# Kernel optimization log

Measured on AMD Instinct MI355X. Metric: run time of the kernel, lower is better.

The kernel has to match this reference:

```python
import jax, jax.numpy as jnp
import numpy as np

B, N, NB, E, H, A, K, D = 32, 512, 10, 1024, 256, 82, 4, 3


def setup_inputs() -> dict:
    key = jax.random.key(0)
    ks = iter(jax.random.split(key, 64))
    f = lambda shape: jax.random.normal(next(ks), shape, jnp.float32) * 0.05
    inp = {
        "atom_fea": jax.random.normal(next(ks), (B, N, A), jnp.float32),
        "bond_fea": jax.random.normal(next(ks), (B, E, 6), jnp.float32),
        "d_anb": jax.random.randint(next(ks), (B, N, NB), 0, N),
        "d_bnb": jax.random.randint(next(ks), (B, N, NB), 0, E),
        "d_nbs_mask": (jax.random.uniform(next(ks), (B, N, NB)) < 0.8).astype(jnp.float32),
        "d_mask": (jax.random.uniform(next(ks), (B, N)) < 0.9).astype(jnp.float32),
        "Wv": f((A, H)), "bv": f((H,)),
        "Wa_main": f((D, K, H, H)), "ba_main": f((D, K, H)),
        "Wa_super": f((D, K, H, H)), "ba_super": f((D, K, H)),
        "Wm": f((D, K, H, H)), "bm": f((D, K, H)),
        "Wbmm": f((D, K, H)), "bbmm": f((D, K)),
        "Wm2s": f((D, K * H, H)), "bm2s": f((D, H)),
        "Ws2m": f((D, H, H)), "bs2m": f((D, H)),
        "Wsup": f((D, H, H)), "bsup": f((D, H)),
        "Wzm1": f((D, H, H)), "bzm1": f((D, H)),
        "Wzm2": f((D, H, H)), "bzm2": f((D, H)),
        "Wzs1": f((D, H, H)), "bzs1": f((D, H)),
        "Wzs2": f((D, H, H)), "bzs2": f((D, H)),
        "Wu2": f((D, H + 6, H)), "bu2": f((D, H)),
        "Wu1": f((D, 2 * H, H)), "bu1": f((D, H)),
    }
    return inp


def mask_softmax(a, mask):
    a_max = jnp.max(a, -1, keepdims=True)
    e = jnp.exp(a - a_max) * mask
    return e / (jnp.sum(e, -1, keepdims=True) + 1e-6)


def _forward(atom_fea, bond_fea, d_nbs_mask, d_mask,
             Wv, bv, Wa_main, ba_main, Wa_super, ba_super, Wm, bm, Wbmm, bbmm,
             Wm2s, bm2s, Ws2m, bs2m, Wsup, bsup,
             Wzm1, bzm1, Wzm2, bzm2, Wzs1, bzs1, Wzs2, bzs2,
             Wu2, bu2, Wu1, bu1, d_anb, d_bnb):
    Bn = atom_fea.shape[0]
    bidx = jnp.arange(Bn)[:, None, None]
    # vertex embedding (default leaky_relu slope 0.01)
    vf = jax.nn.leaky_relu(atom_fea @ Wv + bv, 0.01)            # [B,N,H]
    sf = jnp.sum(vf * d_mask[:, :, None], axis=1, keepdims=True)  # [B,1,H]
    mask3 = d_nbs_mask[..., None]                               # [B,N,NB,1]
    for d in range(D):
        # --- multi-head main->super attention (vectorized over heads k) ---
        a_main = jnp.tanh(jnp.einsum('bnh,khj->bknj', vf, Wa_main[d]) + ba_main[d][None, :, None, :])
        a_super = jnp.tanh(jnp.einsum('boh,khj->bkoj', sf, Wa_super[d]) + ba_super[d][None, :, None, :])
        a = jnp.einsum('bknh,kh->bkn', a_main * a_super, Wbmm[d]) + bbmm[d][None, :, None]
        attn = mask_softmax(a, d_mask[:, None, :])               # [B,K,N]
        mvf = jnp.einsum('bnh,khj->bknj', vf, Wm[d]) + bm[d][None, :, None, :]
        m2s = jnp.einsum('bkn,bknh->bkh', attn, mvf).reshape(Bn, 1, K * H)
        main_to_super = jnp.tanh(m2s @ Wm2s[d] + bm2s[d])        # [B,1,H]
        # --- wln unit: gather neighbors, MLP, masked sum (slope 0.1) ---
        vnei = vf[bidx, d_anb]                                   # [B,N,NB,H]
        enei = bond_fea[bidx, d_bnb]                             # [B,N,NB,6]
        lnei = jnp.concatenate([vnei, enei], -1)                 # [B,N,NB,H+6]
        nei = jax.nn.leaky_relu(lnei @ Wu2[d] + bu2[d], 0.1)
        nei = jnp.sum(nei * mask3, axis=2)                       # [B,N,H]
        main_self = jax.nn.leaky_relu(jnp.concatenate([vf, nei], -1) @ Wu1[d] + bu1[d], 0.1)
        # --- GRU-style gated updates ---
        super_to_main = jnp.tanh(sf @ Ws2m[d] + bs2m[d])         # [B,1,H]
        super_self = jnp.tanh(sf @ Wsup[d] + bsup[d])            # [B,1,H]
        z_main = jax.nn.sigmoid(main_self @ Wzm1[d] + bzm1[d] + super_to_main @ Wzm2[d] + bzm2[d])
        vf = (1 - z_main) * main_self + z_main * super_to_main
        z_sup = jax.nn.sigmoid(super_self @ Wzs1[d] + bzs1[d] + main_to_super @ Wzs2[d] + bzs2[d])
        sf = (1 - z_sup) * super_self + z_sup * main_to_super    # [B,1,H]; sum over dim 1 is a no-op
    return vf, sf


def reference(atom_fea, bond_fea, d_anb, d_bnb, d_nbs_mask, d_mask,
              Wv, bv, Wa_main, ba_main, Wa_super, ba_super, Wm, bm, Wbmm, bbmm,
              Wm2s, bm2s, Ws2m, bs2m, Wsup, bsup,
              Wzm1, bzm1, Wzm2, bzm2, Wzs1, bzs1, Wzs2, bzs2,
              Wu2, bu2, Wu1, bu1):
    return _forward(atom_fea, bond_fea, d_nbs_mask, d_mask,
                    Wv, bv, Wa_main, ba_main, Wa_super, ba_super, Wm, bm, Wbmm, bbmm,
                    Wm2s, bm2s, Ws2m, bs2m, Wsup, bsup,
                    Wzm1, bzm1, Wzm2, bzm2, Wzs1, bzs1, Wzs2, bzs2,
                    Wu2, bu2, Wu1, bu1, d_anb, d_bnb)
```

## Files before the change

kernel.cpp:

```cpp
#include <hip/hip_runtime.h>
#include <hip/hip_bf16.h>

#define B_ 32
#define N_ 512
#define NB_ 10
#define E_ 1024
#define H_ 256
#define A_ 82
#define K_ 4
#define D_ 3
#define M_ (B_*N_)

typedef unsigned short u16;
typedef __attribute__((ext_vector_type(8))) short bf16x8;
typedef __attribute__((ext_vector_type(4))) float f32x4;

__device__ __forceinline__ float b2f(u16 u){
    unsigned int x = ((unsigned int)u) << 16;
    return __builtin_bit_cast(float, x);
}
__device__ __forceinline__ u16 f2b(float f){
    unsigned int x = __builtin_bit_cast(unsigned int, f);
    unsigned int lsb = (x >> 16) & 1u;
    x += 0x7fffu + lsb;
    return (u16)(x >> 16);
}
__device__ __forceinline__ float sigmoidf_(float x){ return 1.f/(1.f+expf(-x)); }

static constexpr int CVT_N[31] = {
    B_*E_*6, B_*N_*NB_, B_*N_,
    A_*H_, H_,
    D_*K_*H_*H_, D_*K_*H_, D_*K_*H_*H_, D_*K_*H_,
    D_*K_*H_*H_, D_*K_*H_, D_*K_*H_, D_*K_,
    D_*K_*H_*H_, D_*H_, D_*H_*H_, D_*H_,
    D_*H_*H_, D_*H_, D_*H_*H_, D_*H_,
    D_*H_*H_, D_*H_, D_*H_*H_, D_*H_,
    D_*H_*H_, D_*H_, D_*(H_+6)*H_, D_*H_,
    D_*2*H_*H_, D_*H_
};
struct Offs { long v[32]; };
static constexpr Offs mk_offs(){
    Offs o{}; o.v[0]=0;
    for(int i=0;i<31;i++) o.v[i+1]=o.v[i]+CVT_N[i];
    return o;
}
static constexpr Offs CVT_OFF = mk_offs();

struct Ptrs { const void* p[31]; };

__global__ void k_detect(const unsigned short* __restrict__ wv_raw, int* __restrict__ flag){
    float v = b2f(wv_raw[threadIdx.x]);
    bool plaus = (v==v) && (fabsf(v) < 100.0f);
    unsigned long long m = __ballot(plaus);
    if (threadIdx.x==0) *flag = (m == ~0ULL) ? 1 : 0;
}

__global__ void k_cvt(Ptrs ptrs, float* __restrict__ dst, const int* __restrict__ flag){
    int t = blockIdx.y;
    int n = CVT_N[t];
    int i4 = blockIdx.x*256 + threadIdx.x;
    if (i4*4 >= n) return;
    const void* src = ptrs.p[t];
    float4 o;
    if (*flag){
        ushort4 u = ((const ushort4*)src)[i4];
        o.x=b2f(u.x); o.y=b2f(u.y); o.z=b2f(u.z); o.w=b2f(u.w);
    } else {
        o = ((const float4*)src)[i4];
    }
    *(float4*)(dst + CVT_OFF.v[t] + (size_t)i4*4) = o;
}

__global__ void k_wt(const float* __restrict__ Wam, const float* __restrict__ Wu2,
                     const float* __restrict__ Wu1, const float* __restrict__ Wzm1,
                     u16* __restrict__ WT){
    int mi = blockIdx.z;
    const float* src;
    if (mi<12)      src = Wam  + (size_t)mi*H_*H_;
    else if (mi<15) src = Wu2  + (size_t)(mi-12)*(H_+6)*H_;
    else if (mi<18) src = Wu1  + (size_t)(mi-15)*2*H_*H_;
    else if (mi<21) src = Wu1  + (size_t)(mi-18)*2*H_*H_ + (size_t)H_*H_;
    else            src = Wzm1 + (size_t)(mi-21)*H_*H_;
    __shared__ float t[32][33];
    int x = threadIdx.x, y = threadIdx.y;
    int k0 = blockIdx.y*32, n0 = blockIdx.x*32;
    for(int yy=y; yy<32; yy+=8) t[yy][x] = src[(size_t)(k0+yy)*H_ + n0+x];
    __syncthreads();
    u16* dst = WT + ((size_t)mi*8 + (k0>>5))*(256*32);
    for(int yy=y; yy<32; yy+=8) dst[(size_t)(n0+yy)*32 + x] = f2b(t[x][yy]);
}

__global__ void k_embed(const u16* __restrict__ atom, const float* __restrict__ Wv,
                        const float* __restrict__ bv, u16* __restrict__ vfb,
                        const int* __restrict__ flag){
    __shared__ float arow[8][A_];
    int r0 = blockIdx.x*8; int j = threadIdx.x;
    int fl = *flag;
    for(int i=j;i<8*A_;i+=256){
        int r=i/A_, a=i-r*A_;
        arow[r][a] = fl ? b2f(atom[(size_t)(r0+r)*A_+a])
                        : ((const float*)atom)[(size_t)(r0+r)*A_+a];
    }
    __syncthreads();
    float acc[8];
    float bj = bv[j];
    #pragma unroll
    for(int r=0;r<8;r++) acc[r]=bj;
    for(int a=0;a<A_;a++){
        float w = Wv[a*H_+j];
        #pragma unroll
        for(int r=0;r<8;r++) acc[r] += arow[r][a]*w;
    }
    #pragma unroll
    for(int r=0;r<8;r++){
        float v = acc[r];
        vfb[(size_t)(r0+r)*H_+j] = f2b(v>0.f ? v : 0.01f*v);
    }
}

__global__ void k_sf0(const u16* __restrict__ vfb, const float* __restrict__ dmask,
                      float* __restrict__ sf){
    int b = blockIdx.x, h = threadIdx.x;
    __shared__ float mk[N_];
    for(int n=threadIdx.x;n<N_;n+=256) mk[n] = dmask[b*N_+n];
    __syncthreads();
    float s=0.f;
    #pragma unroll 8
    for(int n=0;n<N_;n++) s += mk[n]*b2f(vfb[((size_t)b*N_+n)*H_ + h]);
    sf[b*H_+h]=s;
}

__global__ void k_s1(int d, const float* __restrict__ sf,
    const float* __restrict__ Was, const float* __restrict__ bas,
    const float* __restrict__ Wbmm,
    const float* __restrict__ Ws2m, const float* __restrict__ bs2m,
    const float* __restrict__ Wsup, const float* __restrict__ bsup,
    float* __restrict__ asw, float* __restrict__ s2m, float* __restrict__ ssf)
{
    int b = blockIdx.x, m = blockIdx.y, j = threadIdx.x;
    __shared__ float sfl[H_];
    sfl[j] = sf[b*H_+j];
    __syncthreads();
    const float* W; float bias;
    if (m < 4){ W = Was + (size_t)(d*K_+m)*H_*H_; bias = bas[(d*K_+m)*H_+j]; }
    else if (m==4){ W = Ws2m + (size_t)d*H_*H_; bias = bs2m[d*H_+j]; }
    else { W = Wsup + (size_t)d*H_*H_; bias = bsup[d*H_+j]; }
    float acc = bias;
    #pragma unroll 8
    for(int h=0;h<H_;h++) acc += sfl[h]*W[h*H_+j];
    float v = tanhf(acc);
    if (m < 4) asw[(b*K_+m)*H_+j] = v * Wbmm[(d*K_+m)*H_+j];
    else if (m==4) s2m[b*H_+j] = v;
    else ssf[b*H_+j] = v;
}

__global__ void k_s2(int d, const float* __restrict__ s2m,
    const float* __restrict__ Wzm2, const float* __restrict__ bzm2,
    float* __restrict__ stm2p)
{
    int b=blockIdx.x, c=blockIdx.y, j=threadIdx.x;
    __shared__ float xl[64];
    if (j<64) xl[j] = s2m[b*H_ + c*64 + j];
    __syncthreads();
    const float* W = Wzm2 + (size_t)d*H_*H_ + (size_t)(c*64)*H_;
    float acc = (c==0) ? bzm2[d*H_+j] : 0.f;
    #pragma unroll 8
    for(int h=0;h<64;h++) acc += xl[h]*W[h*H_+j];
    stm2p[((size_t)c*B_+b)*H_+j] = acc;
}

__device__ __forceinline__ void mfma_core_bt(const u16* __restrict__ A,
    const u16* __restrict__ WTg, f32x4 acc[2][8],
    u16* __restrict__ Als, u16* __restrict__ Ws)
{
    const int LSA = 40, LSW = 40;
    int tid = threadIdx.x;
    int lane = tid & 63, wave = tid >> 6;
    int wy = wave >> 1, wx = wave & 1;
    int quad = lane >> 4, l15 = lane & 15;
    #pragma unroll
    for(int mt=0;mt<2;mt++)
        #pragma unroll
        for(int nt=0;nt<8;nt++) acc[mt][nt] = (f32x4){0.f,0.f,0.f,0.f};
    int arow = tid >> 2;
    int ak8  = (tid & 3) * 8;
    for(int k0=0;k0<H_;k0+=32){
        *(bf16x8*)(Als + arow*LSA + ak8) =
            *(const bf16x8*)(A + (size_t)arow*H_ + k0 + ak8);
        const u16* wsrc = WTg + (size_t)(k0>>5)*(256*32) + tid*32;
        #pragma unroll
        for(int c=0;c<4;c++)
            *(bf16x8*)(Ws + tid*LSW + c*8) = *(const bf16x8*)(wsrc + c*8);
        __syncthreads();
        bf16x8 af[2], bfr[8];
        #pragma unroll
        for(int mt=0;mt<2;mt++)
            af[mt] = *(const bf16x8*)(Als + (wy*32+mt*16+l15)*LSA + quad*8);
        #pragma unroll
        for(int nt=0;nt<8;nt++)
            bfr[nt] = *(const bf16x8*)(Ws + (wx*128+nt*16+l15)*LSW + quad*8);
        #pragma unroll
        for(int mt=0;mt<2;mt++)
            #pragma unroll
            for(int nt=0;nt<8;nt++)
                acc[mt][nt] = __builtin_amdgcn_mfma_f32_16x16x32_bf16(
                    af[mt], bfr[nt], acc[mt][nt], 0,0,0);
        __syncthreads();
    }
}

__global__ __launch_bounds__(256) void k_gemm_big(int d, const u16* __restrict__ vfb,
    const u16* __restrict__ WT, const float* __restrict__ ba_main,
    const float* __restrict__ bbmm, const float* __restrict__ bu1,
    const float* __restrict__ asw, float* __restrict__ score,
    u16* __restrict__ projb, float* __restrict__ pu1a)
{
    __shared__ u16 Als[64*40];
    __shared__ u16 Ws[256*40];
    __shared__ float sred[64][33];
    int m0 = blockIdx.x*64;
    int seg = blockIdx.y;
    int b = m0 >> 9;
    int mi;
    if (seg < 4)      mi = d*4+seg;
    else if (seg==4)  mi = 12+d;
    else              mi = 15+d;
    f32x4 acc[2][8];
    mfma_core_bt(vfb + (size_t)m0*H_, WT + (size_t)mi*H_*H_, acc, Als, Ws);
    int tid=threadIdx.x, lane=tid&63, wave=tid>>6;
    int wy=wave>>1, wx=wave&1, quad=lane>>4, l15=lane&15;
    if (seg < 4){
        const float* aswp = asw + (size_t)(b*K_+seg)*H_;
        const float* bap  = ba_main + (size_t)(d*K_+seg)*H_;
        float bbv[8], awv[8];
        #pragma unroll
        for(int nt=0;nt<8;nt++){
            int col = wx*128+nt*16+l15;
            bbv[nt]=bap[col]; awv[nt]=aswp[col];
        }
        #pragma unroll
        for(int mt=0;mt<2;mt++)
            #pragma unroll
            for(int r=0;r<4;r++){
                float p=0.f;
                #pragma unroll
                for(int nt=0;nt<8;nt++)
                    p += tanhf(acc[mt][nt][r]+bbv[nt])*awv[nt];
                int row = wy*32+mt*16+quad*4+r;
                sred[row][wx*16+l15] = p;
            }
        __syncthreads();
        if (tid < 64){
            float s=0.f;
            #pragma unroll 8
            for(int i=0;i<32;i++) s += sred[tid][i];
            score[(size_t)(b*K_+seg)*N_ + (m0&511) + tid] = s + bbmm[d*K_+seg];
        }
    } else if (seg==4){
        #pragma unroll
        for(int mt=0;mt<2;mt++)
            #pragma unroll
            for(int nt=0;nt<8;nt++){
                int col = wx*128+nt*16+l15;
                #pragma unroll
                for(int r=0;r<4;r++){
                    int row = m0 + wy*32+mt*16+quad*4+r;
                    projb[(size_t)row*H_+col] = f2b(acc[mt][nt][r]);
                }
            }
    } else {
        const float* bp = bu1 + d*H_;
        #pragma unroll
        for(int mt=0;mt<2;mt++)
            #pragma unroll
            for(int nt=0;nt<8;nt++){
                int col = wx*128+nt*16+l15;
                float bb = bp[col];
                #pragma unroll
                for(int r=0;r<4;r++){
                    int row = m0 + wy*32+mt*16+quad*4+r;
                    pu1a[(size_t)row*H_+col] = acc[mt][nt][r] + bb;
                }
            }
    }
}

#define LSA2_ 264
__global__ __launch_bounds__(256) void k_wln(int d,
    const int* __restrict__ anb, const int* __restrict__ bnb,
    const float* __restrict__ nbm, const float* __restrict__ bond,
    const float* __restrict__ Wu2, const float* __restrict__ bu2,
    const u16* __restrict__ projb, const float* __restrict__ pu1a,
    const u16* __restrict__ WT, const float* __restrict__ bzm1,
    const float* __restrict__ stm2p, const float* __restrict__ s2m,
    u16* __restrict__ vfb)
{
    __shared__ u16 Als[64*LSA2_];
    __shared__ float W2s[6][256];
    __shared__ int   ai[64*NB_];
    __shared__ float mk[64*NB_];
    __shared__ float bfeat[64*NB_][6];
    int m0 = blockIdx.x*64; int b = m0>>9;
    int tid = threadIdx.x;
    {
        const float* W2 = Wu2 + (size_t)d*(H_+6)*H_ + (size_t)H_*H_;
        for(int i=tid;i<6*H_;i+=256) W2s[i>>8][i&255] = W2[i];
    }
    __shared__ int bi[64*NB_];
    for(int i=tid;i<64*NB_;i+=256){
        ai[i]=anb[(size_t)m0*NB_+i]; bi[i]=bnb[(size_t)m0*NB_+i]; mk[i]=nbm[(size_t)m0*NB_+i];
    }
    __syncthreads();
    for(int l=tid;l<64*NB_*6;l+=256){
        int e=l/6, i=l-e*6;
        bfeat[e][i] = bond[((size_t)b*E_+bi[e])*6+i];
    }
    __syncthreads();
    {
        int h = tid;
        float bu = bu2[d*H_+h];
        for(int r=0;r<64;r++){
            float acc=0.f;
            #pragma unroll
            for(int jn=0;jn<NB_;jn++){
                int e=r*NB_+jn;
                float v = b2f(projb[((size_t)b*N_+ai[e])*H_+h]) + bu;
                #pragma unroll
                for(int i=0;i<6;i++) v += bfeat[e][i]*W2s[i][h];
                v = v>0.f? v : 0.1f*v;
                acc += mk[e]*v;
            }
            Als[r*LSA2_+h]=f2b(acc);
        }
    }
    __syncthreads();
    int lane=tid&63, wave=tid>>6, wy=wave>>1, wx=wave&1, quad=lane>>4, l15=lane&15;
    f32x4 acc[2][8];
    {
        const u16* WTg = WT + (size_t)(18+d)*H_*H_;
        #pragma unroll
        for(int mt=0;mt<2;mt++)
            #pragma unroll
            for(int nt=0;nt<8;nt++) acc[mt][nt] = (f32x4){0.f,0.f,0.f,0.f};
        #pragma unroll
        for(int k0=0;k0<H_;k0+=32){
            bf16x8 af[2], bfr[8];
            #pragma unroll
            for(int mt=0;mt<2;mt++)
                af[mt] = *(const bf16x8*)(Als + (wy*32+mt*16+l15)*LSA2_ + k0 + quad*8);
            const u16* wsrc = WTg + (size_t)(k0>>5)*(256*32);
            #pragma unroll
            for(int nt=0;nt<8;nt++)
                bfr[nt] = *(const bf16x8*)(wsrc + (wx*128+nt*16+l15)*32 + quad*8);
            #pragma unroll
            for(int mt=0;mt<2;mt++)
                #pragma unroll
                for(int nt=0;nt<8;nt++)
                    acc[mt][nt] = __builtin_amdgcn_mfma_f32_16x16x32_bf16(
                        af[mt], bfr[nt], acc[mt][nt], 0,0,0);
        }
    }
    __syncthreads();
    #pragma unroll
    for(int mt=0;mt<2;mt++)
        #pragma unroll
        for(int nt=0;nt<8;nt++){
            int col = wx*128+nt*16+l15;
            #pragma unroll
            for(int r=0;r<4;r++){
                int row = wy*32+mt*16+quad*4+r;
                float v = acc[mt][nt][r] + pu1a[(size_t)(m0+row)*H_+col];
                v = v>0.f? v : 0.1f*v;
                Als[row*LSA2_+col] = f2b(v);
            }
        }
    __syncthreads();
    {
        const u16* WTg = WT + (size_t)(21+d)*H_*H_;
        #pragma unroll
        for(int mt=0;mt<2;mt++)
            #pragma unroll
            for(int nt=0;nt<8;nt++) acc[mt][nt] = (f32x4){0.f,0.f,0.f,0.f};
        #pragma unroll
        for(int k0=0;k0<H_;k0+=32){
            bf16x8 af[2], bfr[8];
            #pragma unroll
            for(int mt=0;mt<2;mt++)
                af[mt] = *(const bf16x8*)(Als + (wy*32+mt*16+l15)*LSA2_ + k0 + quad*8);
            const u16* wsrc = WTg + (size_t)(k0>>5)*(256*32);
            #pragma unroll
            for(int nt=0;nt<8;nt++)
                bfr[nt] = *(const bf16x8*)(wsrc + (wx*128+nt*16+l15)*32 + quad*8);
            #pragma unroll
            for(int mt=0;mt<2;mt++)
                #pragma unroll
                for(int nt=0;nt<8;nt++)
                    acc[mt][nt] = __builtin_amdgcn_mfma_f32_16x16x32_bf16(
                        af[mt], bfr[nt], acc[mt][nt], 0,0,0);
        }
    }
    #pragma unroll
    for(int mt=0;mt<2;mt++)
        #pragma unroll
        for(int nt=0;nt<8;nt++){
            int col = wx*128+nt*16+l15;
            float bz = bzm1[d*H_+col];
            float st = stm2p[(size_t)(0*B_+b)*H_+col] + stm2p[(size_t)(1*B_+b)*H_+col]
                     + stm2p[(size_t)(2*B_+b)*H_+col] + stm2p[(size_t)(3*B_+b)*H_+col];
            float sm = s2m[b*H_+col];
            #pragma unroll
            for(int r=0;r<4;r++){
                int row = wy*32+mt*16+quad*4+r;
                float z = sigmoidf_(acc[mt][nt][r] + bz + st);
                float ms = b2f(Als[row*LSA2_+col]);
                vfb[(size_t)(m0+row)*H_+col] = f2b((1.f-z)*ms + z*sm);
            }
        }
}

__global__ void k_softmax(float* __restrict__ score, const float* __restrict__ dmask,
                          float* __restrict__ sumattn){
    int b = blockIdx.x, k = blockIdx.y;
    int tid = threadIdx.x;
    __shared__ float sh[256];
    float* a = score + (size_t)(b*K_+k)*N_;
    float v0 = a[tid], v1 = a[tid+256];
    sh[tid]=fmaxf(v0,v1); __syncthreads();
    for(int s=128;s>0;s>>=1){ if(tid<s) sh[tid]=fmaxf(sh[tid],sh[tid+s]); __syncthreads(); }
    float m = sh[0]; __syncthreads();
    float e0 = expf(v0-m)*dmask[b*N_+tid], e1 = expf(v1-m)*dmask[b*N_+tid+256];
    sh[tid]=e0+e1; __syncthreads();
    for(int s=128;s>0;s>>=1){ if(tid<s) sh[tid]+=sh[tid+s]; __syncthreads(); }
    float S = sh[0];
    float inv = 1.f/(S+1e-6f);
    a[tid]=e0*inv; a[tid+256]=e1*inv;
    if(tid==0) sumattn[b*K_+k]=S*inv;
}

__global__ void k_t2(const float* __restrict__ attn, const u16* __restrict__ vfb,
                     float* __restrict__ tpart){
    int b=blockIdx.x, k=blockIdx.y, c=blockIdx.z, h=threadIdx.x;
    __shared__ float at[256];
    at[h] = attn[(size_t)(b*K_+k)*N_ + c*256 + h];
    __syncthreads();
    float acc=0.f;
    const u16* vfp = vfb + ((size_t)b*N_ + c*256)*H_ + h;
    #pragma unroll 8
    for(int n=0;n<256;n++) acc += at[n]*b2f(vfp[(size_t)n*H_]);
    tpart[((size_t)(c*B_+b)*K_+k)*H_+h]=acc;
}

__global__ void k_m12(int d, const float* __restrict__ tpart, const float* __restrict__ sumattn,
    const float* __restrict__ Wm, const float* __restrict__ bm,
    const float* __restrict__ Wm2s, float* __restrict__ mtsp)
{
    int b=blockIdx.x, k=blockIdx.y, j=threadIdx.x;
    __shared__ float tl[H_];
    __shared__ float m2sl[H_];
    tl[j] = tpart[((size_t)(0*B_+b)*K_+k)*H_+j] + tpart[((size_t)(1*B_+b)*K_+k)*H_+j];
    __syncthreads();
    {
        const float* W = Wm + (size_t)(d*K_+k)*H_*H_;
        float acc = sumattn[b*K_+k]*bm[(d*K_+k)*H_+j];
        #pragma unroll 8
        for(int h=0;h<H_;h++) acc += tl[h]*W[h*H_+j];
        m2sl[j]=acc;
    }
    __syncthreads();
    {
        const float* W = Wm2s + (size_t)d*(K_*H_)*H_ + (size_t)(k*H_)*H_;
        float acc=0.f;
        #pragma unroll 8
        for(int h=0;h<H_;h++) acc += m2sl[h]*W[h*H_+j];
        mtsp[((size_t)k*B_+b)*H_+j]=acc;
    }
}

__global__ void k_sftail(int d, const float* __restrict__ mtsp, const float* __restrict__ bm2s,
    const float* __restrict__ ssf,
    const float* __restrict__ Wzs1, const float* __restrict__ bzs1,
    const float* __restrict__ Wzs2, const float* __restrict__ bzs2,
    float* __restrict__ sf)
{
    int b=blockIdx.x, j=threadIdx.x;
    __shared__ float mtsl[H_];
    __shared__ float ssl[H_];
    {
        float acc = bm2s[d*H_+j];
        #pragma unroll
        for(int c=0;c<4;c++) acc += mtsp[((size_t)c*B_+b)*H_+j];
        mtsl[j]=tanhf(acc);
        ssl[j]=ssf[b*H_+j];
    }
    __syncthreads();
    const float* W1 = Wzs1 + (size_t)d*H_*H_;
    const float* W2 = Wzs2 + (size_t)d*H_*H_;
    float acc = bzs1[d*H_+j] + bzs2[d*H_+j];
    #pragma unroll 4
    for(int h=0;h<H_;h++) acc += ssl[h]*W1[h*H_+j] + mtsl[h]*W2[h*H_+j];
    float z = sigmoidf_(acc);
    sf[b*H_+j]=(1.f-z)*ssl[j]+z*mtsl[j];
}

__global__ void k_out(const u16* __restrict__ vfb, const float* __restrict__ sf,
                      void* __restrict__ out, const int* __restrict__ flag){
    int idx = blockIdx.x*256 + threadIdx.x;
    const int total = M_*H_ + B_*H_;
    if (idx >= total) return;
    if (*flag){
        ((u16*)out)[idx] = (idx < M_*H_) ? vfb[idx] : f2b(sf[idx - M_*H_]);
    } else {
        ((float*)out)[idx] = (idx < M_*H_) ? b2f(vfb[idx]) : sf[idx - M_*H_];
    }
}

extern "C" void kernel_launch(void* const* d_in, const int* in_sizes, int n_in,
                              void* d_out, int out_size, void* d_ws, size_t ws_size,
                              hipStream_t stream)
{
    const int* anb = (const int*)d_in[2];
    const int* bnb = (const int*)d_in[3];

    float* ws   = (float*)d_ws;
    int*   flag = (int*)ws;
    float* cvt  = ws + 64;
    float* p    = cvt + ((CVT_OFF.v[31] + 63) & ~63L);
    float* pu1a      = p; p += (size_t)M_*H_;
    float* sf        = p; p += B_*H_;
    float* score     = p; p += B_*K_*N_;
    float* sumattn   = p; p += 128;
    float* asw       = p; p += B_*K_*H_;
    float* s2m       = p; p += B_*H_;
    float* ssf       = p; p += B_*H_;
    float* stm2p     = p; p += 4*B_*H_;
    float* tpart     = p; p += 2*B_*K_*H_;
    float* mtsp      = p; p += 4*B_*H_;
    u16*   WT        = (u16*)p;
    u16*   vfb       = WT  + (size_t)24*H_*H_;
    u16*   projb     = vfb + (size_t)M_*H_;

    const float* cBond = cvt + CVT_OFF.v[0];
    const float* cNbm  = cvt + CVT_OFF.v[1];
    const float* cDm   = cvt + CVT_OFF.v[2];
    const float* cWv   = cvt + CVT_OFF.v[3];
    const float* cbv   = cvt + CVT_OFF.v[4];
    const float* cWam  = cvt + CVT_OFF.v[5];
    const float* cbam  = cvt + CVT_OFF.v[6];
    const float* cWas  = cvt + CVT_OFF.v[7];
    const float* cbas  = cvt + CVT_OFF.v[8];
    const float* cWm   = cvt + CVT_OFF.v[9];
    const float* cbm   = cvt + CVT_OFF.v[10];
    const float* cWbmm = cvt + CVT_OFF.v[11];
    const float* cbbmm = cvt + CVT_OFF.v[12];
    const float* cWm2s = cvt + CVT_OFF.v[13];
    const float* cbm2s = cvt + CVT_OFF.v[14];
    const float* cWs2m = cvt + CVT_OFF.v[15];
    const float* cbs2m = cvt + CVT_OFF.v[16];
    const float* cWsup = cvt + CVT_OFF.v[17];
    const float* cbsup = cvt + CVT_OFF.v[18];
    const float* cWzm1 = cvt + CVT_OFF.v[19];
    const float* cbzm1 = cvt + CVT_OFF.v[20];
    const float* cWzm2 = cvt + CVT_OFF.v[21];
    const float* cbzm2 = cvt + CVT_OFF.v[22];
    const float* cWzs1 = cvt + CVT_OFF.v[23];
    const float* cbzs1 = cvt + CVT_OFF.v[24];
    const float* cWzs2 = cvt + CVT_OFF.v[25];
    const float* cbzs2 = cvt + CVT_OFF.v[26];
    const float* cWu2  = cvt + CVT_OFF.v[27];
    const float* cbu2  = cvt + CVT_OFF.v[28];
    const float* cWu1  = cvt + CVT_OFF.v[29];
    const float* cbu1  = cvt + CVT_OFF.v[30];

    Ptrs ptrs;
    {
        int idx[31] = {1,4,5,6,7,8,9,10,11,12,13,14,15,16,17,18,19,20,21,
                       22,23,24,25,26,27,28,29,30,31,32,33};
        for(int i=0;i<31;i++) ptrs.p[i] = d_in[idx[i]];
    }

    k_detect<<<1,64,0,stream>>>((const unsigned short*)d_in[6], flag);
    {
        int maxv4 = (D_*K_*H_*H_ + 3)/4;
        int gx = (maxv4 + 255)/256;
        k_cvt<<<dim3(gx,31),256,0,stream>>>(ptrs, cvt, flag);
    }
    k_wt<<<dim3(8,8,24),dim3(32,8),0,stream>>>(cWam, cWu2, cWu1, cWzm1, WT);

    k_embed<<<M_/8,256,0,stream>>>((const u16*)d_in[0], cWv, cbv, vfb, flag);
    k_sf0<<<B_,256,0,stream>>>(vfb, cDm, sf);
    for(int d=0; d<D_; d++){
        k_s1<<<dim3(B_,6),256,0,stream>>>(d, sf, cWas, cbas, cWbmm,
                                          cWs2m, cbs2m, cWsup, cbsup, asw, s2m, ssf);
        k_s2<<<dim3(B_,4),256,0,stream>>>(d, s2m, cWzm2, cbzm2, stm2p);
        k_gemm_big<<<dim3(M_/64,6),256,0,stream>>>(d, vfb, WT, cbam, cbbmm, cbu1,
                                                   asw, score, projb, pu1a);
        k_softmax<<<dim3(B_,K_),256,0,stream>>>(score, cDm, sumattn);
        k_t2<<<dim3(B_,K_,2),256,0,stream>>>(score, vfb, tpart);
        k_m12<<<dim3(B_,K_),256,0,stream>>>(d, tpart, sumattn, cWm, cbm, cWm2s, mtsp);
        k_sftail<<<B_,256,0,stream>>>(d, mtsp, cbm2s, ssf, cWzs1, cbzs1,
                                      cWzs2, cbzs2, sf);
        k_wln<<<M_/64,256,0,stream>>>(d, anb, bnb, cNbm, cBond, cWu2, cbu2,
                                      projb, pu1a, WT, cbzm1, stm2p, s2m, vfb);
    }
    k_out<<<(M_*H_+B_*H_+255)/256,256,0,stream>>>(vfb, sf, d_out, flag);
}
```

Baseline: 760.5 us.

## Split neighbor aggregation out of k_wln into a per-row kernel

The fused k_wln kernel is split in two. A new k_nei kernel does the neighbor gather, bond projection and masked leaky-relu sum with one block per atom row, and writes the result to a new bf16 buffer. k_msupd then loads that buffer into shared memory for the MFMA GEMM and gated update. The gather phase had only 256 blocks, each doing a serial 64-row loop, so this spreads it across far more blocks. The cost is an extra kernel launch, a global round trip for the intermediate, and reloading the W2 weights in every one of the many small blocks.

```diff
diff --git a/kernel.cpp b/kernel.cpp
--- a/kernel.cpp
+++ b/kernel.cpp
@@ -285,56 +285,52 @@
     }
 }
 
-#define LSA2_ 264
-__global__ __launch_bounds__(256) void k_wln(int d,
-    const int* __restrict__ anb, const int* __restrict__ bnb,
+__global__ void k_nei(int d, const int* __restrict__ anb, const int* __restrict__ bnb,
     const float* __restrict__ nbm, const float* __restrict__ bond,
     const float* __restrict__ Wu2, const float* __restrict__ bu2,
-    const u16* __restrict__ projb, const float* __restrict__ pu1a,
-    const u16* __restrict__ WT, const float* __restrict__ bzm1,
-    const float* __restrict__ stm2p, const float* __restrict__ s2m,
-    u16* __restrict__ vfb)
+    const u16* __restrict__ projb, u16* __restrict__ neib)
+{
+    __shared__ float W2s[6][256];
+    __shared__ float bfeat[NB_][6];
+    __shared__ int ai[NB_]; __shared__ int bi[NB_]; __shared__ float mk[NB_];
+    int row = blockIdx.x; int b = row >> 9; int h = threadIdx.x;
+    const float* W2 = Wu2 + (size_t)d*(H_+6)*H_ + (size_t)H_*H_;
+    for(int i=h;i<6*H_;i+=256) W2s[i>>8][i&255] = W2[i];
+    if (h<NB_){ ai[h]=anb[row*NB_+h]; bi[h]=bnb[row*NB_+h]; mk[h]=nbm[row*NB_+h]; }
+    __syncthreads();
+    if (h<NB_*6){ int jn=h/6, i=h-jn*6; bfeat[jn][i]=bond[((size_t)b*E_+bi[jn])*6+i]; }
+    __syncthreads();
+    float bu = bu2[d*H_+h];
+    float acc=0.f;
+    #pragma unroll
+    for(int jn=0;jn<NB_;jn++){
+        float v = b2f(projb[((size_t)b*N_+ai[jn])*H_+h]) + bu;
+        #pragma unroll
+        for(int i=0;i<6;i++) v += bfeat[jn][i]*W2s[i][h];
+        v = v>0.f? v : 0.1f*v;
+        acc += mk[jn]*v;
+    }
+    neib[(size_t)row*H_+h]=f2b(acc);
+}
+
+#define LSA2_ 264
+__global__ __launch_bounds__(256) void k_msupd(int d, const u16* __restrict__ neib,
+    const float* __restrict__ pu1a, const u16* __restrict__ WT,
+    const float* __restrict__ bzm1, const float* __restrict__ stm2p,
+    const float* __restrict__ s2m, u16* __restrict__ vfb)
 {
     __shared__ u16 Als[64*LSA2_];
-    __shared__ float W2s[6][256];
-    __shared__ int   ai[64*NB_];
-    __shared__ float mk[64*NB_];
-    __shared__ float bfeat[64*NB_][6];
     int m0 = blockIdx.x*64; int b = m0>>9;
     int tid = threadIdx.x;
-    {
-        const float* W2 = Wu2 + (size_t)d*(H_+6)*H_ + (size_t)H_*H_;
-        for(int i=tid;i<6*H_;i+=256) W2s[i>>8][i&255] = W2[i];
-    }
-    __shared__ int bi[64*NB_];
-    for(int i=tid;i<64*NB_;i+=256){
-        ai[i]=anb[(size_t)m0*NB_+i]; bi[i]=bnb[(size_t)m0*NB_+i]; mk[i]=nbm[(size_t)m0*NB_+i];
-    }
-    __syncthreads();
-    for(int l=tid;l<64*NB_*6;l+=256){
-        int e=l/6, i=l-e*6;
-        bfeat[e][i] = bond[((size_t)b*E_+bi[e])*6+i];
-    }
-    __syncthreads();
-    {
-        int h = tid;
-        float bu = bu2[d*H_+h];
-        for(int r=0;r<64;r++){
-            float acc=0.f;
-            #pragma unroll
-            for(int jn=0;jn<NB_;jn++){
-                int e=r*NB_+jn;
-                float v = b2f(projb[((size_t)b*N_+ai[e])*H_+h]) + bu;
-                #pragma unroll
-                for(int i=0;i<6;i++) v += bfeat[e][i]*W2s[i][h];
-                v = v>0.f? v : 0.1f*v;
-                acc += mk[e]*v;
-            }
-            Als[r*LSA2_+h]=f2b(acc);
-        }
-    }
-    __syncthreads();
     int lane=tid&63, wave=tid>>6, wy=wave>>1, wx=wave&1, quad=lane>>4, l15=lane&15;
+    {
+        int arow = tid>>2, ac=(tid&3)*8;
+        #pragma unroll
+        for(int c=0;c<8;c++)
+            *(bf16x8*)(Als + arow*LSA2_ + ac + c*32) =
+                *(const bf16x8*)(neib + (size_t)(m0+arow)*H_ + ac + c*32);
+    }
+    __syncthreads();
     f32x4 acc[2][8];
     {
         const u16* WTg = WT + (size_t)(18+d)*H_*H_;
@@ -538,6 +534,7 @@
     u16*   WT        = (u16*)p;
     u16*   vfb       = WT  + (size_t)24*H_*H_;
     u16*   projb     = vfb + (size_t)M_*H_;
+    u16*   neib      = projb + (size_t)M_*H_;
 
     const float* cBond = cvt + CVT_OFF.v[0];
     const float* cNbm  = cvt + CVT_OFF.v[1];
@@ -599,8 +596,8 @@
         k_m12<<<dim3(B_,K_),256,0,stream>>>(d, tpart, sumattn, cWm, cbm, cWm2s, mtsp);
         k_sftail<<<B_,256,0,stream>>>(d, mtsp, cbm2s, ssf, cWzs1, cbzs1,
                                       cWzs2, cbzs2, sf);
-        k_wln<<<M_/64,256,0,stream>>>(d, anb, bnb, cNbm, cBond, cWu2, cbu2,
-                                      projb, pu1a, WT, cbzm1, stm2p, s2m, vfb);
+        k_nei<<<M_,256,0,stream>>>(d, anb, bnb, cNbm, cBond, cWu2, cbu2, projb, neib);
+        k_msupd<<<M_/64,256,0,stream>>>(d, neib, pu1a, WT, cbzm1, stm2p, s2m, vfb);
     }
     k_out<<<(M_*H_+B_*H_+255)/256,256,0,stream>>>(vfb, sf, d_out, flag);
 }
```

Measured after the change: 779.6 us. +2.5%, slower.

## Precompute per-bond projection and halve wln row tile to 32

Applied to the files above, without the earlier changes.

Adds a k_bondproj kernel that computes bond_fea @ Wu2_tail + bu2 once per bond (B*E rows) as bf16, so k_wln gathers a precomputed vector instead of redoing a 6-term dot product for every neighbour. k_wln's row tile drops from 64 to 32, which doubles the block count (more parallelism, fewer rows per block) and removes the W2s and bfeat shared buffers. The cost is an extra kernel launch per layer, an extra B*E*H bf16 buffer to write and gather, added bf16 rounding on the bond term, and weight tiles reloaded per 32 rows instead of per 64.

```diff
diff --git a/kernel.cpp b/kernel.cpp
--- a/kernel.cpp
+++ b/kernel.cpp
@@ -285,48 +285,58 @@
     }
 }
 
+__global__ void k_bondproj(int d, const float* __restrict__ bond,
+    const float* __restrict__ Wu2, const float* __restrict__ bu2,
+    u16* __restrict__ bproj)
+{
+    __shared__ float W2s[6][256];
+    __shared__ float bfl[8][6];
+    int r0 = blockIdx.x*8;
+    int j = threadIdx.x;
+    const float* W2 = Wu2 + (size_t)d*(H_+6)*H_ + (size_t)H_*H_;
+    for(int i=j;i<6*H_;i+=256) W2s[i>>8][i&255] = W2[i];
+    if (j<48){ int r=j/6, i=j-r*6; bfl[r][i]=bond[(size_t)(r0+r)*6+i]; }
+    __syncthreads();
+    float bu = bu2[d*H_+j];
+    #pragma unroll
+    for(int r=0;r<8;r++){
+        float acc = bu;
+        #pragma unroll
+        for(int i=0;i<6;i++) acc += bfl[r][i]*W2s[i][j];
+        bproj[(size_t)(r0+r)*H_+j] = f2b(acc);
+    }
+}
+
+#define TM_ 32
 #define LSA2_ 264
 __global__ __launch_bounds__(256) void k_wln(int d,
     const int* __restrict__ anb, const int* __restrict__ bnb,
-    const float* __restrict__ nbm, const float* __restrict__ bond,
-    const float* __restrict__ Wu2, const float* __restrict__ bu2,
-    const u16* __restrict__ projb, const float* __restrict__ pu1a,
+    const float* __restrict__ nbm,
+    const u16* __restrict__ bproj, const u16* __restrict__ projb,
+    const float* __restrict__ pu1a,
     const u16* __restrict__ WT, const float* __restrict__ bzm1,
     const float* __restrict__ stm2p, const float* __restrict__ s2m,
     u16* __restrict__ vfb)
 {
-    __shared__ u16 Als[64*LSA2_];
-    __shared__ float W2s[6][256];
-    __shared__ int   ai[64*NB_];
-    __shared__ float mk[64*NB_];
-    __shared__ float bfeat[64*NB_][6];
-    int m0 = blockIdx.x*64; int b = m0>>9;
+    __shared__ u16 Als[TM_*LSA2_];
+    __shared__ int   ai[TM_*NB_];
+    __shared__ int   bi[TM_*NB_];
+    __shared__ float mk[TM_*NB_];
+    int m0 = blockIdx.x*TM_; int b = m0>>9;
     int tid = threadIdx.x;
-    {
-        const float* W2 = Wu2 + (size_t)d*(H_+6)*H_ + (size_t)H_*H_;
-        for(int i=tid;i<6*H_;i+=256) W2s[i>>8][i&255] = W2[i];
-    }
-    __shared__ int bi[64*NB_];
-    for(int i=tid;i<64*NB_;i+=256){
+    for(int i=tid;i<TM_*NB_;i+=256){
         ai[i]=anb[(size_t)m0*NB_+i]; bi[i]=bnb[(size_t)m0*NB_+i]; mk[i]=nbm[(size_t)m0*NB_+i];
     }
     __syncthreads();
-    for(int l=tid;l<64*NB_*6;l+=256){
-        int e=l/6, i=l-e*6;
-        bfeat[e][i] = bond[((size_t)b*E_+bi[e])*6+i];
-    }
-    __syncthreads();
     {
         int h = tid;
-        float bu = bu2[d*H_+h];
-        for(int r=0;r<64;r++){
+        for(int r=0;r<TM_;r++){
             float acc=0.f;
             #pragma unroll
             for(int jn=0;jn<NB_;jn++){
                 int e=r*NB_+jn;
-                float v = b2f(projb[((size_t)b*N_+ai[e])*H_+h]) + bu;
-                #pragma unroll
-                for(int i=0;i<6;i++) v += bfeat[e][i]*W2s[i][h];
+                float v = b2f(projb[((size_t)b*N_+ai[e])*H_+h])
+                        + b2f(bproj[((size_t)b*E_+bi[e])*H_+h]);
                 v = v>0.f? v : 0.1f*v;
                 acc += mk[e]*v;
             }
@@ -335,87 +345,65 @@
     }
     __syncthreads();
     int lane=tid&63, wave=tid>>6, wy=wave>>1, wx=wave&1, quad=lane>>4, l15=lane&15;
-    f32x4 acc[2][8];
+    f32x4 acc[8];
     {
         const u16* WTg = WT + (size_t)(18+d)*H_*H_;
         #pragma unroll
-        for(int mt=0;mt<2;mt++)
-            #pragma unroll
-            for(int nt=0;nt<8;nt++) acc[mt][nt] = (f32x4){0.f,0.f,0.f,0.f};
+        for(int nt=0;nt<8;nt++) acc[nt]=(f32x4){0.f,0.f,0.f,0.f};
         #pragma unroll
         for(int k0=0;k0<H_;k0+=32){
-            bf16x8 af[2], bfr[8];
-            #pragma unroll
-            for(int mt=0;mt<2;mt++)
-                af[mt] = *(const bf16x8*)(Als + (wy*32+mt*16+l15)*LSA2_ + k0 + quad*8);
+            bf16x8 af = *(const bf16x8*)(Als + (wy*16+l15)*LSA2_ + k0 + quad*8);
             const u16* wsrc = WTg + (size_t)(k0>>5)*(256*32);
             #pragma unroll
-            for(int nt=0;nt<8;nt++)
-                bfr[nt] = *(const bf16x8*)(wsrc + (wx*128+nt*16+l15)*32 + quad*8);
-            #pragma unroll
-            for(int mt=0;mt<2;mt++)
-                #pragma unroll
-                for(int nt=0;nt<8;nt++)
-                    acc[mt][nt] = __builtin_amdgcn_mfma_f32_16x16x32_bf16(
-                        af[mt], bfr[nt], acc[mt][nt], 0,0,0);
+            for(int nt=0;nt<8;nt++){
+                bf16x8 bfr = *(const bf16x8*)(wsrc + (wx*128+nt*16+l15)*32 + quad*8);
+                acc[nt]=__builtin_amdgcn_mfma_f32_16x16x32_bf16(af,bfr,acc[nt],0,0,0);
+            }
         }
     }
     __syncthreads();
     #pragma unroll
-    for(int mt=0;mt<2;mt++)
-        #pragma unroll
-        for(int nt=0;nt<8;nt++){
-            int col = wx*128+nt*16+l15;
-            #pragma unroll
-            for(int r=0;r<4;r++){
-                int row = wy*32+mt*16+quad*4+r;
-                float v = acc[mt][nt][r] + pu1a[(size_t)(m0+row)*H_+col];
-                v = v>0.f? v : 0.1f*v;
-                Als[row*LSA2_+col] = f2b(v);
+    for(int nt=0;nt<8;nt++){
+        int col = wx*128+nt*16+l15;
+        #pragma unroll
+        for(int r=0;r<4;r++){
+            int row = wy*16+quad*4+r;
+            float v = acc[nt][r] + pu1a[(size_t)(m0+row)*H_+col];
+            v = v>0.f? v : 0.1f*v;
+            Als[row*LSA2_+col] = f2b(v);
+        }
+    }
+    __syncthreads();
+    {
+        const u16* WTg = WT + (size_t)(21+d)*H_*H_;
+        #pragma unroll
+        for(int nt=0;nt<8;nt++) acc[nt]=(f32x4){0.f,0.f,0.f,0.f};
+        #pragma unroll
+        for(int k0=0;k0<H_;k0+=32){
+            bf16x8 af = *(const bf16x8*)(Als + (wy*16+l15)*LSA2_ + k0 + quad*8);
+            const u16* wsrc = WTg + (size_t)(k0>>5)*(256*32);
+            #pragma unroll
+            for(int nt=0;nt<8;nt++){
+                bf16x8 bfr = *(const bf16x8*)(wsrc + (wx*128+nt*16+l15)*32 + quad*8);
+                acc[nt]=__builtin_amdgcn_mfma_f32_16x16x32_bf16(af,bfr,acc[nt],0,0,0);
             }
         }
-    __syncthreads();
-    {
-        const u16* WTg = WT + (size_t)(21+d)*H_*H_;
-        #pragma unroll
-        for(int mt=0;mt<2;mt++)
-            #pragma unroll
-            for(int nt=0;nt<8;nt++) acc[mt][nt] = (f32x4){0.f,0.f,0.f,0.f};
-        #pragma unroll
-        for(int k0=0;k0<H_;k0+=32){
-            bf16x8 af[2], bfr[8];
-            #pragma unroll
-            for(int mt=0;mt<2;mt++)
-                af[mt] = *(const bf16x8*)(Als + (wy*32+mt*16+l15)*LSA2_ + k0 + quad*8);
-            const u16* wsrc = WTg + (size_t)(k0>>5)*(256*32);
-            #pragma unroll
-            for(int nt=0;nt<8;nt++)
-                bfr[nt] = *(const bf16x8*)(wsrc + (wx*128+nt*16+l15)*32 + quad*8);
-            #pragma unroll
-            for(int mt=0;mt<2;mt++)
-                #pragma unroll
-                for(int nt=0;nt<8;nt++)
-                    acc[mt][nt] = __builtin_amdgcn_mfma_f32_16x16x32_bf16(
-                        af[mt], bfr[nt], acc[mt][nt], 0,0,0);
-        }
     }
     #pragma unroll
-    for(int mt=0;mt<2;mt++)
-        #pragma unroll
-        for(int nt=0;nt<8;nt++){
-            int col = wx*128+nt*16+l15;
-            float bz = bzm1[d*H_+col];
-            float st = stm2p[(size_t)(0*B_+b)*H_+col] + stm2p[(size_t)(1*B_+b)*H_+col]
-                     + stm2p[(size_t)(2*B_+b)*H_+col] + stm2p[(size_t)(3*B_+b)*H_+col];
-            float sm = s2m[b*H_+col];
-            #pragma unroll
-            for(int r=0;r<4;r++){
-                int row = wy*32+mt*16+quad*4+r;
-                float z = sigmoidf_(acc[mt][nt][r] + bz + st);
-                float ms = b2f(Als[row*LSA2_+col]);
-                vfb[(size_t)(m0+row)*H_+col] = f2b((1.f-z)*ms + z*sm);
-            }
-        }
+    for(int nt=0;nt<8;nt++){
+        int col = wx*128+nt*16+l15;
+        float bz = bzm1[d*H_+col];
+        float st = stm2p[(size_t)(0*B_+b)*H_+col] + stm2p[(size_t)(1*B_+b)*H_+col]
+                 + stm2p[(size_t)(2*B_+b)*H_+col] + stm2p[(size_t)(3*B_+b)*H_+col];
+        float sm = s2m[b*H_+col];
+        #pragma unroll
+        for(int r=0;r<4;r++){
+            int row = wy*16+quad*4+r;
+            float z = sigmoidf_(acc[nt][r] + bz + st);
+            float ms = b2f(Als[row*LSA2_+col]);
+            vfb[(size_t)(m0+row)*H_+col] = f2b((1.f-z)*ms + z*sm);
+        }
+    }
 }
 
 __global__ void k_softmax(float* __restrict__ score, const float* __restrict__ dmask,
@@ -538,6 +526,7 @@
     u16*   WT        = (u16*)p;
     u16*   vfb       = WT  + (size_t)24*H_*H_;
     u16*   projb     = vfb + (size_t)M_*H_;
+    u16*   bproj     = projb + (size_t)M_*H_;
 
     const float* cBond = cvt + CVT_OFF.v[0];
     const float* cNbm  = cvt + CVT_OFF.v[1];
@@ -592,6 +581,7 @@
         k_s1<<<dim3(B_,6),256,0,stream>>>(d, sf, cWas, cbas, cWbmm,
                                           cWs2m, cbs2m, cWsup, cbsup, asw, s2m, ssf);
         k_s2<<<dim3(B_,4),256,0,stream>>>(d, s2m, cWzm2, cbzm2, stm2p);
+        k_bondproj<<<B_*E_/8,256,0,stream>>>(d, cBond, cWu2, cbu2, bproj);
         k_gemm_big<<<dim3(M_/64,6),256,0,stream>>>(d, vfb, WT, cbam, cbbmm, cbu1,
                                                    asw, score, projb, pu1a);
         k_softmax<<<dim3(B_,K_),256,0,stream>>>(score, cDm, sumattn);
@@ -599,8 +589,8 @@
         k_m12<<<dim3(B_,K_),256,0,stream>>>(d, tpart, sumattn, cWm, cbm, cWm2s, mtsp);
         k_sftail<<<B_,256,0,stream>>>(d, mtsp, cbm2s, ssf, cWzs1, cbzs1,
                                       cWzs2, cbzs2, sf);
-        k_wln<<<M_/64,256,0,stream>>>(d, anb, bnb, cNbm, cBond, cWu2, cbu2,
-                                      projb, pu1a, WT, cbzm1, stm2p, s2m, vfb);
+        k_wln<<<M_/TM_,256,0,stream>>>(d, anb, bnb, cNbm, bproj, projb,
+                                       pu1a, WT, cbzm1, stm2p, s2m, vfb);
     }
     k_out<<<(M_*H_+B_*H_+255)/256,256,0,stream>>>(vfb, sf, d_out, flag);
 }
```

After: 811.5 us. 6.7% more time.
